# Performance work log

Hardware: AMD Instinct MI355X
Metric: run time of the kernel (lower is better)

The kernel has to match this reference:

```python
import jax, jax.numpy as jnp
import numpy as np

BATCH, D_MODEL, N_STATE, SEQ_L = 8, 1024, 64, 2048


def setup_inputs() -> dict:
    key = jax.random.key(0)
    k_u, k_a, k_b, k_c = jax.random.split(key, 4)
    scale = 1.0 / (D_MODEL * N_STATE) ** 0.5
    u = jax.random.normal(k_u, (BATCH, D_MODEL, SEQ_L), dtype=jnp.float32)
    # A is stored as a full NxN diagonal matrix, as in the torch module
    A = jnp.diag(jax.random.uniform(k_a, (N_STATE,), dtype=jnp.float32))
    B = jax.random.normal(k_b, (D_MODEL, N_STATE), dtype=jnp.float32) * scale
    C = jax.random.normal(k_c, (D_MODEL, N_STATE), dtype=jnp.float32) * scale
    return {"L": SEQ_L, "u": u, "A": A, "B": B, "C": C}


def reference(L, u, A, B, C):
    # u: (B, D, L). einsum('nn,bnd->bnd', A, h) in torch == diag(A) broadcast over h.
    a = jnp.diagonal(A)                       # (N,)
    Bu = jnp.einsum('dn,bdl->bnl', B, u)      # (B, N, L)
    Cu = jnp.einsum('dn,bdl->bnl', C, u)      # (B, N, L)
    bsz, d, _ = u.shape
    h0 = jnp.zeros((bsz, a.shape[0], d), dtype=u.dtype)  # (B, N, D)

    def step(h, xs):
        bu_l, cu_l, u_l = xs                  # (B,N), (B,N), (B,D)
        h = a[None, :, None] * h + bu_l[:, :, None] * u_l[:, None, :]
        y_l = jnp.einsum('bn,bnd->bd', cu_l, h)
        return h, y_l

    xs = (jnp.moveaxis(Bu, -1, 0), jnp.moveaxis(Cu, -1, 0), jnp.moveaxis(u, -1, 0))
    _, ys = jax.lax.scan(step, h0, xs)        # ys: (L, B, D)
    return jnp.moveaxis(ys, 0, -1)            # (B, D, L)
```

## Files before the change

kernel.cpp:

```cpp
#include <hip/hip_runtime.h>
#include <hip/hip_bf16.h>
#include <string.h>

#define BATCH 8
#define DM 1024
#define NS 64
#define SL 2048
#define NC 32
#define TC 64

typedef __attribute__((ext_vector_type(8))) short bf16x8;
typedef __attribute__((ext_vector_type(4))) float f32x4;
typedef float v2f __attribute__((ext_vector_type(2)));

__device__ inline unsigned short f2bf(float f) {
    union { float f; unsigned u; } v; v.f = f;
    return (unsigned short)((v.u + 0x7fffu + ((v.u >> 16) & 1u)) >> 16);
}
__device__ inline float bf2f(unsigned short h) {
    return __uint_as_float(((unsigned)h) << 16);
}
static __device__ inline v2f bfpair_to_v2f(unsigned int p) {
    unsigned int lo = p << 16, hi = p & 0xffff0000u;
    v2f r; r.x = __uint_as_float(lo); r.y = __uint_as_float(hi); return r;
}


__global__ __launch_bounds__(256) void k_prep(const float* __restrict__ Bm,
                                              const float* __restrict__ Cm,
                                              unsigned short* __restrict__ BT,
                                              unsigned short* __restrict__ CT)
{
    __shared__ float sT[64][65];
    const float* src = blockIdx.y ? Cm : Bm;
    unsigned short* dst = blockIdx.y ? CT : BT;
    const int d0 = blockIdx.x * 64, t = threadIdx.x;
    {
        int r = t >> 2, f = (t & 3) * 16;
#pragma unroll
        for (int i = 0; i < 4; i++) {
            float4 v = *(const float4*)&src[(size_t)(d0 + r) * NS + f + i * 4];
            sT[r][f + i * 4 + 0] = v.x; sT[r][f + i * 4 + 1] = v.y;
            sT[r][f + i * 4 + 2] = v.z; sT[r][f + i * 4 + 3] = v.w;
        }
    }
    __syncthreads();
    {
        int n = t >> 2, dq = (t & 3) * 16;
        unsigned pk[8];
#pragma unroll
        for (int k = 0; k < 8; k++) {
            unsigned short a = f2bf(sT[dq + 2 * k][n]);
            unsigned short bb = f2bf(sT[dq + 2 * k + 1][n]);
            pk[k] = (unsigned)a | ((unsigned)bb << 16);
        }
        uint4 v0 = { pk[0], pk[1], pk[2], pk[3] };
        uint4 v1 = { pk[4], pk[5], pk[6], pk[7] };
        *(uint4*)&dst[(size_t)n * DM + d0 + dq] = v0;
        *(uint4*)&dst[(size_t)n * DM + d0 + dq + 8] = v1;
    }
}

__global__ __launch_bounds__(256) void k_proj(const float* __restrict__ u,
                                              const unsigned short* __restrict__ BC,
                                              unsigned short* __restrict__ BuT,
                                              unsigned short* __restrict__ CuT)
{
    __shared__ unsigned short sA[32 * 64];
    __shared__ unsigned short sB[128 * 64];
    const int b = blockIdx.y, l0 = blockIdx.x * 32, t = threadIdx.x;
    const int lane = t & 63, w = t >> 6, g = lane >> 4, m15 = lane & 15;

    f32x4 acc[2][2];
#pragma unroll
    for (int i = 0; i < 2; i++)
#pragma unroll
        for (int j = 0; j < 2; j++) acc[i][j] = (f32x4){0.f, 0.f, 0.f, 0.f};

#pragma unroll 1
    for (int d0 = 0; d0 < DM; d0 += 64) {
        __syncthreads();
#pragma unroll
        for (int p = 0; p < 2; p++) {
            int dd = p * 32 + (t >> 3), f = t & 7;
            float4 v = *(const float4*)&u[((size_t)b * DM + d0 + dd) * SL + l0 + f * 4];
            int l = f * 4;
            sA[(l + 0) * 64 + (((dd >> 3) ^ ((l + 0) & 7)) * 8) + (dd & 7)] = f2bf(v.x);
            sA[(l + 1) * 64 + (((dd >> 3) ^ ((l + 1) & 7)) * 8) + (dd & 7)] = f2bf(v.y);
            sA[(l + 2) * 64 + (((dd >> 3) ^ ((l + 2) & 7)) * 8) + (dd & 7)] = f2bf(v.z);
            sA[(l + 3) * 64 + (((dd >> 3) ^ ((l + 3) & 7)) * 8) + (dd & 7)] = f2bf(v.w);
        }
#pragma unroll
        for (int p = 0; p < 4; p++) {
            int row = p * 32 + (t >> 3), c8 = t & 7;
            uint4 v = *(const uint4*)(BC + (size_t)row * DM + d0 + c8 * 8);
            *(uint4*)&sB[row * 64 + ((c8 ^ (row & 7)) * 8)] = v;
        }
        __syncthreads();
#pragma unroll
        for (int ks = 0; ks < 2; ks++) {
            bf16x8 af[2], bf[2];
#pragma unroll
            for (int mt = 0; mt < 2; mt++) {
                int r = mt * 16 + m15;
                af[mt] = *(const bf16x8*)&sA[r * 64 + (((ks * 4 + g) ^ (r & 7)) * 8)];
            }
#pragma unroll
            for (int nt = 0; nt < 2; nt++) {
                int r = w * 32 + nt * 16 + m15;
                bf[nt] = *(const bf16x8*)&sB[r * 64 + (((ks * 4 + g) ^ (r & 7)) * 8)];
            }
#pragma unroll
            for (int mt = 0; mt < 2; mt++)
#pragma unroll
                for (int nt = 0; nt < 2; nt++)
                    acc[mt][nt] = __builtin_amdgcn_mfma_f32_16x16x32_bf16(af[mt], bf[nt], acc[mt][nt], 0, 0, 0);
        }
    }
#pragma unroll
    for (int mt = 0; mt < 2; mt++)
#pragma unroll
        for (int nt = 0; nt < 2; nt++) {
            int wn = w * 32 + nt * 16 + m15;
            unsigned short* dst = (wn < 64) ? BuT : CuT;
            int n = wn & 63;
#pragma unroll
            for (int r = 0; r < 4; r++) {
                int l = l0 + mt * 16 + g * 4 + r;
                dst[((size_t)b * SL + l) * NS + n] = f2bf(acc[mt][nt][r]);
            }
        }
}

__global__ __launch_bounds__(256) void k_g(const float* __restrict__ A,
                                           const unsigned short* __restrict__ BuT,
                                           const unsigned short* __restrict__ CuT,
                                           unsigned short* __restrict__ Gw,
                                           unsigned short* __restrict__ Bvw,
                                           unsigned short* __restrict__ Wcw)
{
    __shared__ unsigned short sCu[64 * 64];
    __shared__ unsigned short sBu[8 * 64 * 8];
    __shared__ unsigned short sP[8 * 66 * 8];
    __shared__ unsigned short sTb[64 * 66];
    const int cc = blockIdx.x, b = cc >> 5, c = cc & 31;
    const int t = threadIdx.x, lane = t & 63;
    const int l0 = c * TC;
    const size_t gbase = (size_t)cc * 4096;

    {
        const unsigned short* srcC = CuT + ((size_t)b * SL + l0) * NS;
        const unsigned short* srcB = BuT + ((size_t)b * SL + l0) * NS;
#pragma unroll
        for (int p = 0; p < 2; p++) {
            int idx = p * 256 + t;
            int r = idx >> 3, q8 = idx & 7;
            uint4 vc = *(const uint4*)(srcC + (size_t)r * NS + q8 * 8);
            *(uint4*)&sCu[r * 64 + q8 * 8] = vc;
            uint4 vb = *(const uint4*)(srcB + (size_t)r * NS + q8 * 8);
            *(uint4*)&sBu[(q8 * 64 + r) * 8] = vb;
        }
    }
    {
        int n = t & 63;
        float an = A[n * NS + n];
        int q = n >> 3, n7 = n & 7;
#pragma unroll 1
        for (int dl = (t >> 6) * 17; dl < (t >> 6) * 17 + 17 && dl <= 64; dl++)
            sP[(q * 66 + dl) * 8 + n7] = f2bf(__powf(an, (float)dl));
    }
    __syncthreads();

#pragma unroll 1
    for (int r = 0; r < 16; r++) {
        int idx = r * 256 + t;
        int l = idx >> 6;
        int lp = lane;
        int dl = l - lp;
        float acc = 0.f;
        if (dl >= 0) {
#pragma unroll
            for (int q = 0; q < 8; q++) {
                bf16x8 cu = *(const bf16x8*)&sCu[l * 64 + q * 8];
                bf16x8 bu = *(const bf16x8*)&sBu[(q * 64 + lp) * 8];
                bf16x8 pp = *(const bf16x8*)&sP[(q * 66 + dl) * 8];
#pragma unroll
                for (int j = 0; j < 8; j++)
                    acc = fmaf(bf2f((unsigned short)cu[j]) * bf2f((unsigned short)bu[j]),
                               bf2f((unsigned short)pp[j]), acc);
            }
        }
        Gw[gbase + l * 64 + lp] = (dl >= 0) ? f2bf(acc) : (unsigned short)0;
    }

#pragma unroll 1
    for (int r = 0; r < 16; r++) {
        int idx = r * 256 + t;
        int l = idx >> 6;
        int n = lane, q = n >> 3, n7 = n & 7;
        float cu = bf2f(sCu[l * 64 + n]);
        float pv = bf2f(sP[(q * 66 + (l + 1)) * 8 + n7]);
        Wcw[gbase + l * 64 + n] = f2bf(cu * pv);
    }

#pragma unroll 1
    for (int r = 0; r < 16; r++) {
        int idx = r * 256 + t;
        int l = idx >> 6;
        int n = lane, q = n >> 3, n7 = n & 7;
        float bu = bf2f(sBu[(q * 64 + l) * 8 + n7]);
        float pv = bf2f(sP[(q * 66 + (63 - l)) * 8 + n7]);
        sTb[n * 66 + l] = f2bf(bu * pv);
    }
    __syncthreads();
#pragma unroll 1
    for (int r = 0; r < 16; r++) {
        int idx = r * 256 + t;
        int n = idx >> 6;
        int l = lane;
        Bvw[gbase + n * 64 + l] = sTb[n * 66 + l];
    }
}

__global__ __launch_bounds__(256) void k_chunk(const float* __restrict__ u,
                                               const unsigned short* __restrict__ Gw,
                                               const unsigned short* __restrict__ Bvw,
                                               unsigned short* __restrict__ Ew,
                                               float* __restrict__ y)
{
    __shared__ unsigned short sU[256 * 64];
    __shared__ unsigned short sG[64 * 64];
    __shared__ unsigned short sV[64 * 64];
    const int slab = blockIdx.x, c = blockIdx.y, b = blockIdx.z;
    const int d0 = slab * 256, l0 = c * TC;
    const int t = threadIdx.x, lane = t & 63, w = t >> 6, g = lane >> 4, m15 = lane & 15;

    {
        size_t gbase = ((size_t)(b * NC + c)) * 4096;
        int rr = t >> 3, c8 = t & 7;
#pragma unroll
        for (int p = 0; p < 2; p++) {
            int r = p * 32 + rr;
            uint4 gv = *(const uint4*)(Gw + gbase + r * 64 + c8 * 8);
            *(uint4*)&sG[r * 64 + ((c8 ^ (r & 7)) * 8)] = gv;
            uint4 vv = *(const uint4*)(Bvw + gbase + r * 64 + c8 * 8);
            *(uint4*)&sV[r * 64 + ((c8 ^ (r & 7)) * 8)] = vv;
        }
    }
#pragma unroll
    for (int p = 0; p < 16; p++) {
        int dd = p * 16 + (t >> 4), f = t & 15;
        float4 v = *(const float4*)&u[((size_t)b * DM + d0 + dd) * SL + l0 + f * 4];
        unsigned lo = (unsigned)f2bf(v.x) | ((unsigned)f2bf(v.y) << 16);
        unsigned hi = (unsigned)f2bf(v.z) | ((unsigned)f2bf(v.w) << 16);
        uint2 pk = { lo, hi };
        *(uint2*)&sU[dd * 64 + (((f >> 1) ^ (dd & 7)) * 8) + (f & 1) * 4] = pk;
    }
    __syncthreads();

    f32x4 accY[4][4], accE[4][4];
#pragma unroll
    for (int i = 0; i < 4; i++)
#pragma unroll
        for (int j = 0; j < 4; j++) {
            accY[i][j] = (f32x4){0.f, 0.f, 0.f, 0.f};
            accE[i][j] = (f32x4){0.f, 0.f, 0.f, 0.f};
        }

#pragma unroll
    for (int ks = 0; ks < 2; ks++) {
        bf16x8 af[4];
#pragma unroll
        for (int mt = 0; mt < 4; mt++) {
            int r = w * 64 + mt * 16 + m15;
            af[mt] = *(const bf16x8*)&sU[r * 64 + (((ks * 4 + g) ^ (r & 7)) * 8)];
        }
#pragma unroll
        for (int nt = 0; nt < 4; nt++) {
            int rg = nt * 16 + m15;
            bf16x8 bg = *(const bf16x8*)&sG[rg * 64 + (((ks * 4 + g) ^ (rg & 7)) * 8)];
            bf16x8 bv = *(const bf16x8*)&sV[rg * 64 + (((ks * 4 + g) ^ (rg & 7)) * 8)];
#pragma unroll
            for (int mt = 0; mt < 4; mt++) {
                accY[mt][nt] = __builtin_amdgcn_mfma_f32_16x16x32_bf16(af[mt], bg, accY[mt][nt], 0, 0, 0);
                accE[mt][nt] = __builtin_amdgcn_mfma_f32_16x16x32_bf16(af[mt], bv, accE[mt][nt], 0, 0, 0);
            }
        }
    }
#pragma unroll
    for (int mt = 0; mt < 4; mt++)
#pragma unroll
        for (int nt = 0; nt < 4; nt++)
#pragma unroll
            for (int r = 0; r < 4; r++) {
                int d = d0 + w * 64 + mt * 16 + g * 4 + r;
                int l = l0 + nt * 16 + m15;
                y[((size_t)b * DM + d) * SL + l] = accY[mt][nt][r];
                Ew[(((size_t)b * NC + c) * DM + d) * NS + nt * 16 + m15] = f2bf(accE[mt][nt][r]);
            }
}

__global__ __launch_bounds__(256) void k_prefix(const float* __restrict__ A,
                                                unsigned short* __restrict__ E)
{
    int gg = blockIdx.x * 256 + threadIdx.x;
    int p  = gg & 31;
    int d  = (gg >> 5) & (DM - 1);
    int b  = gg >> 15;
    int n0 = p * 2;

    float a0 = A[n0 * NS + n0];
    float a1 = A[(n0 + 1) * NS + (n0 + 1)];
    v2f aT = { __powf(a0, (float)TC), __powf(a1, (float)TC) };
    v2f hs = { 0.f, 0.f };

    unsigned int* base = (unsigned int*)E + ((((size_t)b * NC) * DM + d) * NS >> 1) + p;
    const size_t cstride = ((size_t)DM * NS) >> 1;

#pragma unroll 4
    for (int c = 0; c < NC; c++) {
        unsigned int* ptr = base + (size_t)c * cstride;
        unsigned int e = *ptr;
        unsigned int sw = (unsigned)f2bf(hs.x) | ((unsigned)f2bf(hs.y) << 16);
        *ptr = sw;
        hs = __builtin_elementwise_fma(aT, hs, bfpair_to_v2f(e));
    }
}

__global__ __launch_bounds__(256) void k_corr(const unsigned short* __restrict__ Ew,
                                              const unsigned short* __restrict__ Wcw,
                                              float* __restrict__ y)
{
    __shared__ unsigned short sH[256 * 64];
    __shared__ unsigned short sW[64 * 64];
    const int slab = blockIdx.x, c = blockIdx.y + 1, b = blockIdx.z;
    const int d0 = slab * 256, l0 = c * TC;
    const int t = threadIdx.x, lane = t & 63, w = t >> 6, g = lane >> 4, m15 = lane & 15;

    {
        int rr = t >> 3, c8 = t & 7;
#pragma unroll
        for (int p = 0; p < 8; p++) {
            int r = p * 32 + rr;
            uint4 v = *(const uint4*)(Ew + (((size_t)b * NC + c) * DM + d0 + r) * NS + c8 * 8);
            *(uint4*)&sH[r * 64 + ((c8 ^ (r & 7)) * 8)] = v;
        }
        size_t wbase = ((size_t)(b * NC + c)) * 4096;
#pragma unroll
        for (int p = 0; p < 2; p++) {
            int r = p * 32 + rr;
            uint4 v = *(const uint4*)(Wcw + wbase + r * 64 + c8 * 8);
            *(uint4*)&sW[r * 64 + ((c8 ^ (r & 7)) * 8)] = v;
        }
    }
    __syncthreads();

    f32x4 acc[4][4];
#pragma unroll
    for (int i = 0; i < 4; i++)
#pragma unroll
        for (int j = 0; j < 4; j++) acc[i][j] = (f32x4){0.f, 0.f, 0.f, 0.f};

#pragma unroll
    for (int ks = 0; ks < 2; ks++) {
        bf16x8 af[4];
#pragma unroll
        for (int mt = 0; mt < 4; mt++) {
            int r = w * 64 + mt * 16 + m15;
            af[mt] = *(const bf16x8*)&sH[r * 64 + (((ks * 4 + g) ^ (r & 7)) * 8)];
        }
#pragma unroll
        for (int nt = 0; nt < 4; nt++) {
            int rg = nt * 16 + m15;
            bf16x8 bw = *(const bf16x8*)&sW[rg * 64 + (((ks * 4 + g) ^ (rg & 7)) * 8)];
#pragma unroll
            for (int mt = 0; mt < 4; mt++)
                acc[mt][nt] = __builtin_amdgcn_mfma_f32_16x16x32_bf16(af[mt], bw, acc[mt][nt], 0, 0, 0);
        }
    }
#pragma unroll
    for (int mt = 0; mt < 4; mt++)
#pragma unroll
        for (int nt = 0; nt < 4; nt++)
#pragma unroll
            for (int r = 0; r < 4; r++) {
                int d = d0 + w * 64 + mt * 16 + g * 4 + r;
                int l = l0 + nt * 16 + m15;
                float* p = &y[((size_t)b * DM + d) * SL + l];
                *p = *p + acc[mt][nt][r];
            }
}

extern "C" void kernel_launch(void* const* d_in, const int* in_sizes, int n_in,
                              void* d_out, int out_size, void* d_ws, size_t ws_size,
                              hipStream_t stream) {
    const float* u = (const float*)d_in[1];
    const float* A = (const float*)d_in[2];
    const float* B = (const float*)d_in[3];
    const float* C = (const float*)d_in[4];
    float* y = (float*)d_out;

    char* base = (char*)d_ws;
    unsigned short* BuT = (unsigned short*)(base);
    unsigned short* CuT = (unsigned short*)(base + (2u << 20));
    unsigned short* BT  = (unsigned short*)(base + (4u << 20));
    unsigned short* Gw  = (unsigned short*)(base + (5u << 20));
    unsigned short* Bvw = (unsigned short*)(base + (7u << 20));
    unsigned short* Wcw = (unsigned short*)(base + (9u << 20));
    unsigned short* Ew  = (unsigned short*)(base + (11u << 20));
    unsigned short* CT  = BT + (size_t)NS * DM;

    k_prep<<<dim3(DM / 64, 2), 256, 0, stream>>>(B, C, BT, CT);
    k_proj<<<dim3(SL / 32, BATCH), 256, 0, stream>>>(u, BT, BuT, CuT);
    k_g<<<dim3(BATCH * NC), 256, 0, stream>>>(A, BuT, CuT, Gw, Bvw, Wcw);
    k_chunk<<<dim3(4, NC, BATCH), 256, 0, stream>>>(u, Gw, Bvw, Ew, y);
    k_prefix<<<dim3(BATCH * DM * 32 / 256), 256, 0, stream>>>(A, Ew);
    k_corr<<<dim3(4, NC - 1, BATCH), 256, 0, stream>>>(Ew, Wcw, y);
}
```

Baseline: 121.7 us.

## Move intra-chunk output into final pass, write y once, prefetch proj tiles

The intra-chunk output GEMM (u times G) moves out of the chunk kernel and into the final correction kernel. That kernel now computes the intra-chunk term and the carried-state term together and stores y once, replacing a store followed by a later read-modify-write. The cost is reading u a second time in the final kernel, and chunk 0 is now processed there as well. Separately, k_proj prefetches the next u and B/C tiles into registers while the current tile is being multiplied, hiding global load latency.

```diff
diff --git a/kernel.cpp b/kernel.cpp
--- a/kernel.cpp
+++ b/kernel.cpp
@@ -70,6 +70,15 @@
     __shared__ unsigned short sB[128 * 64];
     const int b = blockIdx.y, l0 = blockIdx.x * 32, t = threadIdx.x;
     const int lane = t & 63, w = t >> 6, g = lane >> 4, m15 = lane & 15;
+    const int rr = t >> 3, c8 = t & 7;
+
+    float4 vU[2]; uint4 vB[4];
+#pragma unroll
+    for (int p = 0; p < 2; p++)
+        vU[p] = *(const float4*)&u[((size_t)b * DM + p * 32 + rr) * SL + l0 + c8 * 4];
+#pragma unroll
+    for (int p = 0; p < 4; p++)
+        vB[p] = *(const uint4*)(BC + (size_t)(p * 32 + rr) * DM + c8 * 8);
 
     f32x4 acc[2][2];
 #pragma unroll
@@ -82,9 +91,8 @@
         __syncthreads();
 #pragma unroll
         for (int p = 0; p < 2; p++) {
-            int dd = p * 32 + (t >> 3), f = t & 7;
-            float4 v = *(const float4*)&u[((size_t)b * DM + d0 + dd) * SL + l0 + f * 4];
-            int l = f * 4;
+            int dd = p * 32 + rr, l = c8 * 4;
+            float4 v = vU[p];
             sA[(l + 0) * 64 + (((dd >> 3) ^ ((l + 0) & 7)) * 8) + (dd & 7)] = f2bf(v.x);
             sA[(l + 1) * 64 + (((dd >> 3) ^ ((l + 1) & 7)) * 8) + (dd & 7)] = f2bf(v.y);
             sA[(l + 2) * 64 + (((dd >> 3) ^ ((l + 2) & 7)) * 8) + (dd & 7)] = f2bf(v.z);
@@ -92,11 +100,18 @@
         }
 #pragma unroll
         for (int p = 0; p < 4; p++) {
-            int row = p * 32 + (t >> 3), c8 = t & 7;
-            uint4 v = *(const uint4*)(BC + (size_t)row * DM + d0 + c8 * 8);
-            *(uint4*)&sB[row * 64 + ((c8 ^ (row & 7)) * 8)] = v;
+            int row = p * 32 + rr;
+            *(uint4*)&sB[row * 64 + ((c8 ^ (row & 7)) * 8)] = vB[p];
         }
         __syncthreads();
+        if (d0 + 64 < DM) {
+#pragma unroll
+            for (int p = 0; p < 2; p++)
+                vU[p] = *(const float4*)&u[((size_t)b * DM + d0 + 64 + p * 32 + rr) * SL + l0 + c8 * 4];
+#pragma unroll
+            for (int p = 0; p < 4; p++)
+                vB[p] = *(const uint4*)(BC + (size_t)(p * 32 + rr) * DM + d0 + 64 + c8 * 8);
+        }
 #pragma unroll
         for (int ks = 0; ks < 2; ks++) {
             bf16x8 af[2], bf[2];
@@ -222,14 +237,11 @@
     }
 }
 
-__global__ __launch_bounds__(256) void k_chunk(const float* __restrict__ u,
-                                               const unsigned short* __restrict__ Gw,
+__global__ __launch_bounds__(256) void k_state(const float* __restrict__ u,
                                                const unsigned short* __restrict__ Bvw,
-                                               unsigned short* __restrict__ Ew,
-                                               float* __restrict__ y)
+                                               unsigned short* __restrict__ Ew)
 {
     __shared__ unsigned short sU[256 * 64];
-    __shared__ unsigned short sG[64 * 64];
     __shared__ unsigned short sV[64 * 64];
     const int slab = blockIdx.x, c = blockIdx.y, b = blockIdx.z;
     const int d0 = slab * 256, l0 = c * TC;
@@ -241,8 +253,6 @@
 #pragma unroll
         for (int p = 0; p < 2; p++) {
             int r = p * 32 + rr;
-            uint4 gv = *(const uint4*)(Gw + gbase + r * 64 + c8 * 8);
-            *(uint4*)&sG[r * 64 + ((c8 ^ (r & 7)) * 8)] = gv;
             uint4 vv = *(const uint4*)(Bvw + gbase + r * 64 + c8 * 8);
             *(uint4*)&sV[r * 64 + ((c8 ^ (r & 7)) * 8)] = vv;
         }
@@ -258,14 +268,11 @@
     }
     __syncthreads();
 
-    f32x4 accY[4][4], accE[4][4];
+    f32x4 accE[4][4];
 #pragma unroll
     for (int i = 0; i < 4; i++)
 #pragma unroll
-        for (int j = 0; j < 4; j++) {
-            accY[i][j] = (f32x4){0.f, 0.f, 0.f, 0.f};
-            accE[i][j] = (f32x4){0.f, 0.f, 0.f, 0.f};
-        }
+        for (int j = 0; j < 4; j++) accE[i][j] = (f32x4){0.f, 0.f, 0.f, 0.f};
 
 #pragma unroll
     for (int ks = 0; ks < 2; ks++) {
@@ -278,13 +285,10 @@
 #pragma unroll
         for (int nt = 0; nt < 4; nt++) {
             int rg = nt * 16 + m15;
-            bf16x8 bg = *(const bf16x8*)&sG[rg * 64 + (((ks * 4 + g) ^ (rg & 7)) * 8)];
             bf16x8 bv = *(const bf16x8*)&sV[rg * 64 + (((ks * 4 + g) ^ (rg & 7)) * 8)];
 #pragma unroll
-            for (int mt = 0; mt < 4; mt++) {
-                accY[mt][nt] = __builtin_amdgcn_mfma_f32_16x16x32_bf16(af[mt], bg, accY[mt][nt], 0, 0, 0);
+            for (int mt = 0; mt < 4; mt++)
                 accE[mt][nt] = __builtin_amdgcn_mfma_f32_16x16x32_bf16(af[mt], bv, accE[mt][nt], 0, 0, 0);
-            }
         }
     }
 #pragma unroll
@@ -294,8 +298,6 @@
 #pragma unroll
             for (int r = 0; r < 4; r++) {
                 int d = d0 + w * 64 + mt * 16 + g * 4 + r;
-                int l = l0 + nt * 16 + m15;
-                y[((size_t)b * DM + d) * SL + l] = accY[mt][nt][r];
                 Ew[(((size_t)b * NC + c) * DM + d) * NS + nt * 16 + m15] = f2bf(accE[mt][nt][r]);
             }
 }
@@ -327,31 +329,39 @@
     }
 }
 
-__global__ __launch_bounds__(256) void k_corr(const unsigned short* __restrict__ Ew,
-                                              const unsigned short* __restrict__ Wcw,
-                                              float* __restrict__ y)
-{
-    __shared__ unsigned short sH[256 * 64];
+__global__ __launch_bounds__(256) void k_y(const float* __restrict__ u,
+                                           const unsigned short* __restrict__ Gw,
+                                           const unsigned short* __restrict__ Wcw,
+                                           const unsigned short* __restrict__ HS,
+                                           float* __restrict__ y)
+{
+    __shared__ unsigned short sU[256 * 64];
+    __shared__ unsigned short sG[64 * 64];
     __shared__ unsigned short sW[64 * 64];
-    const int slab = blockIdx.x, c = blockIdx.y + 1, b = blockIdx.z;
+    const int slab = blockIdx.x, c = blockIdx.y, b = blockIdx.z;
     const int d0 = slab * 256, l0 = c * TC;
     const int t = threadIdx.x, lane = t & 63, w = t >> 6, g = lane >> 4, m15 = lane & 15;
 
     {
+        size_t gbase = ((size_t)(b * NC + c)) * 4096;
         int rr = t >> 3, c8 = t & 7;
-#pragma unroll
-        for (int p = 0; p < 8; p++) {
-            int r = p * 32 + rr;
-            uint4 v = *(const uint4*)(Ew + (((size_t)b * NC + c) * DM + d0 + r) * NS + c8 * 8);
-            *(uint4*)&sH[r * 64 + ((c8 ^ (r & 7)) * 8)] = v;
-        }
-        size_t wbase = ((size_t)(b * NC + c)) * 4096;
 #pragma unroll
         for (int p = 0; p < 2; p++) {
             int r = p * 32 + rr;
-            uint4 v = *(const uint4*)(Wcw + wbase + r * 64 + c8 * 8);
-            *(uint4*)&sW[r * 64 + ((c8 ^ (r & 7)) * 8)] = v;
-        }
+            uint4 gv = *(const uint4*)(Gw + gbase + r * 64 + c8 * 8);
+            *(uint4*)&sG[r * 64 + ((c8 ^ (r & 7)) * 8)] = gv;
+            uint4 wv = *(const uint4*)(Wcw + gbase + r * 64 + c8 * 8);
+            *(uint4*)&sW[r * 64 + ((c8 ^ (r & 7)) * 8)] = wv;
+        }
+    }
+#pragma unroll
+    for (int p = 0; p < 16; p++) {
+        int dd = p * 16 + (t >> 4), f = t & 15;
+        float4 v = *(const float4*)&u[((size_t)b * DM + d0 + dd) * SL + l0 + f * 4];
+        unsigned lo = (unsigned)f2bf(v.x) | ((unsigned)f2bf(v.y) << 16);
+        unsigned hi = (unsigned)f2bf(v.z) | ((unsigned)f2bf(v.w) << 16);
+        uint2 pk = { lo, hi };
+        *(uint2*)&sU[dd * 64 + (((f >> 1) ^ (dd & 7)) * 8) + (f & 1) * 4] = pk;
     }
     __syncthreads();
 
@@ -360,6 +370,8 @@
     for (int i = 0; i < 4; i++)
 #pragma unroll
         for (int j = 0; j < 4; j++) acc[i][j] = (f32x4){0.f, 0.f, 0.f, 0.f};
+
+    const unsigned short* hbase = HS + (((size_t)b * NC + c) * DM + d0) * NS;
 
 #pragma unroll
     for (int ks = 0; ks < 2; ks++) {
@@ -367,7 +379,24 @@
 #pragma unroll
         for (int mt = 0; mt < 4; mt++) {
             int r = w * 64 + mt * 16 + m15;
-            af[mt] = *(const bf16x8*)&sH[r * 64 + (((ks * 4 + g) ^ (r & 7)) * 8)];
+            af[mt] = *(const bf16x8*)&sU[r * 64 + (((ks * 4 + g) ^ (r & 7)) * 8)];
+        }
+#pragma unroll
+        for (int nt = 0; nt < 4; nt++) {
+            int rg = nt * 16 + m15;
+            bf16x8 bg = *(const bf16x8*)&sG[rg * 64 + (((ks * 4 + g) ^ (rg & 7)) * 8)];
+#pragma unroll
+            for (int mt = 0; mt < 4; mt++)
+                acc[mt][nt] = __builtin_amdgcn_mfma_f32_16x16x32_bf16(af[mt], bg, acc[mt][nt], 0, 0, 0);
+        }
+    }
+#pragma unroll
+    for (int ks = 0; ks < 2; ks++) {
+        bf16x8 ah[4];
+#pragma unroll
+        for (int mt = 0; mt < 4; mt++) {
+            int r = w * 64 + mt * 16 + m15;
+            ah[mt] = *(const bf16x8*)(hbase + (size_t)r * NS + (ks * 4 + g) * 8);
         }
 #pragma unroll
         for (int nt = 0; nt < 4; nt++) {
@@ -375,7 +404,7 @@
             bf16x8 bw = *(const bf16x8*)&sW[rg * 64 + (((ks * 4 + g) ^ (rg & 7)) * 8)];
 #pragma unroll
             for (int mt = 0; mt < 4; mt++)
-                acc[mt][nt] = __builtin_amdgcn_mfma_f32_16x16x32_bf16(af[mt], bw, acc[mt][nt], 0, 0, 0);
+                acc[mt][nt] = __builtin_amdgcn_mfma_f32_16x16x32_bf16(ah[mt], bw, acc[mt][nt], 0, 0, 0);
         }
     }
 #pragma unroll
@@ -386,8 +415,7 @@
             for (int r = 0; r < 4; r++) {
                 int d = d0 + w * 64 + mt * 16 + g * 4 + r;
                 int l = l0 + nt * 16 + m15;
-                float* p = &y[((size_t)b * DM + d) * SL + l];
-                *p = *p + acc[mt][nt][r];
+                y[((size_t)b * DM + d) * SL + l] = acc[mt][nt][r];
             }
 }
 
@@ -413,7 +441,7 @@
     k_prep<<<dim3(DM / 64, 2), 256, 0, stream>>>(B, C, BT, CT);
     k_proj<<<dim3(SL / 32, BATCH), 256, 0, stream>>>(u, BT, BuT, CuT);
     k_g<<<dim3(BATCH * NC), 256, 0, stream>>>(A, BuT, CuT, Gw, Bvw, Wcw);
-    k_chunk<<<dim3(4, NC, BATCH), 256, 0, stream>>>(u, Gw, Bvw, Ew, y);
+    k_state<<<dim3(4, NC, BATCH), 256, 0, stream>>>(u, Bvw, Ew);
     k_prefix<<<dim3(BATCH * DM * 32 / 256), 256, 0, stream>>>(A, Ew);
-    k_corr<<<dim3(4, NC - 1, BATCH), 256, 0, stream>>>(Ew, Wcw, y);
-}
+    k_y<<<dim3(4, NC, BATCH), 256, 0, stream>>>(u, Gw, Wcw, Ew, y);
+}
```

New measurement: 133.3 us. 1.1x slower.
